# Kernel tuning notes

Hardware: AMD Instinct MI355X
Metric: run time of the kernel (lower is better)

## Reference

```python
import jax, jax.numpy as jnp
import numpy as np

B, T, I, H, O = 256, 512, 64, 512, 1


def setup_inputs() -> dict:
    key = jax.random.key(0)
    ks = jax.random.split(key, 8)
    s_ih = 1.0 / np.sqrt(H)
    inp = {
        "x": jax.random.normal(ks[0], (B, T, I), dtype=jnp.float32),
        "W_ih": jax.random.uniform(ks[1], (4 * H, I), minval=-s_ih, maxval=s_ih, dtype=jnp.float32),
        "W_hh": jax.random.uniform(ks[2], (4 * H, H), minval=-s_ih, maxval=s_ih, dtype=jnp.float32),
        "b_ih": jax.random.uniform(ks[3], (4 * H,), minval=-s_ih, maxval=s_ih, dtype=jnp.float32),
        "b_hh": jax.random.uniform(ks[4], (4 * H,), minval=-s_ih, maxval=s_ih, dtype=jnp.float32),
        "W_fc": jax.random.uniform(ks[5], (O, H), minval=-s_ih, maxval=s_ih, dtype=jnp.float32),
        "b_fc": jax.random.uniform(ks[6], (O,), minval=-s_ih, maxval=s_ih, dtype=jnp.float32),
    }
    return inp


def _lstm_last_h(x, W_ih, W_hh, b_ih, b_hh):
    # x: [B, T, I]. Precompute input projection for all timesteps (one big GEMM).
    x_gates = jnp.einsum("bti,gi->btg", x, W_ih) + b_ih + b_hh  # [B, T, 4H]
    x_gates = jnp.swapaxes(x_gates, 0, 1)  # [T, B, 4H] for scan
    hdim = W_hh.shape[1]
    h0 = jnp.zeros((x.shape[0], hdim), dtype=x.dtype)
    c0 = jnp.zeros((x.shape[0], hdim), dtype=x.dtype)

    def step(carry, xg):
        h, c = carry
        gates = xg + h @ W_hh.T  # [B, 4H]
        i, f, g, o = jnp.split(gates, 4, axis=-1)  # PyTorch gate order: i, f, g, o
        i = jax.nn.sigmoid(i)
        f = jax.nn.sigmoid(f)
        g = jnp.tanh(g)
        o = jax.nn.sigmoid(o)
        c = f * c + i * g
        h = o * jnp.tanh(c)
        return (h, c), None

    (h_last, _), _ = jax.lax.scan(step, (h0, c0), x_gates)
    return h_last  # [B, H] == out[:, -1, :] for a single-layer LSTM


def reference(x, W_ih, W_hh, b_ih, b_hh, W_fc, b_fc):
    h_last = _lstm_last_h(x, W_ih, W_hh, b_ih, b_hh)
    return h_last @ W_fc.T + b_fc  # [B, O]
```

## Files before the change

### kernel.cpp

```cpp
#include <hip/hip_runtime.h>

typedef _Float16 h8 __attribute__((ext_vector_type(8)));
typedef float v4f __attribute__((ext_vector_type(4)));
typedef unsigned long long u64;

#define B_  256
#define T_  512
#define I_  64
#define H_  512

#define OFF_W16   0
#define OFF_WIH   (OFF_W16 + 2048*512*2)
#define OFF_BIAS  (OFF_WIH + 2048*64*2)
#define OFF_X16   (OFF_BIAS + 2048*4)
#define OFF_H0    (OFF_X16 + 512*256*64*2)
#define OFF_H1    (OFF_H0 + 256*512*2)
#define OFF_CTR   (OFF_H1 + 256*512*2)

#define CS_ 1040

__device__ __forceinline__ float sigf(float x) {
    float e = __builtin_amdgcn_exp2f(-1.442695041f * x);
    return __builtin_amdgcn_rcpf(1.f + e);
}
__device__ __forceinline__ float tanhf_(float x) {
    float e = __builtin_amdgcn_exp2f(2.885390082f * x);
    return 1.f - 2.f * __builtin_amdgcn_rcpf(e + 1.f);
}

union Pack4 { _Float16 f[4]; u64 u; };

__global__ void prep_w(const float* __restrict__ Wih, const float* __restrict__ Whh,
                       const float* __restrict__ bih, const float* __restrict__ bhh,
                       _Float16* __restrict__ W16, _Float16* __restrict__ Wih16,
                       float* __restrict__ bias, _Float16* __restrict__ h0,
                       unsigned* __restrict__ ctr) {
    int idx = blockIdx.x * 256 + threadIdx.x;
    W16[idx] = (_Float16)Whh[idx];
    if (idx < 2048 * 64)  Wih16[idx] = (_Float16)Wih[idx];
    if (idx < 2048)       bias[idx] = bih[idx] + bhh[idx];
    if (idx < 32768)
        __hip_atomic_store((u64*)h0 + idx, 0ull,
                           __ATOMIC_RELAXED, __HIP_MEMORY_SCOPE_AGENT);
    if (idx < 256)
        __hip_atomic_store(ctr + idx, 0u, __ATOMIC_RELAXED, __HIP_MEMORY_SCOPE_AGENT);
}

__global__ void prep_x(const float* __restrict__ x, _Float16* __restrict__ x16) {
    int idx = blockIdx.x * 256 + threadIdx.x;
    int t = idx >> 14;
    int rem = idx & 16383;
    int b = rem >> 6;
    int i = rem & 63;
    x16[idx] = (_Float16)x[((size_t)b * T_ + t) * I_ + i];
}

__launch_bounds__(256, 1)
__global__ void lstm_k(const _Float16* __restrict__ W16, const _Float16* __restrict__ Wih16,
                       const float* __restrict__ bias, const _Float16* __restrict__ x16,
                       _Float16* __restrict__ h0, _Float16* __restrict__ h1,
                       unsigned* __restrict__ ctr) {
    __shared__ __align__(16) char Ab[16 * CS_];

    const int tid  = threadIdx.x;
    const int lane = tid & 63;
    const int wv   = tid >> 6;
    const int bg   = blockIdx.x & 15;
    const int cg   = blockIdx.x >> 4;
    const int B0   = bg * 16;
    const int J0   = cg * 64;
    const int r    = lane & 15;
    const int q    = lane >> 4;

    h8 bfrag[4][16];
    h8 xbfrag[4][2];
    float biasv[4];
#pragma unroll
    for (int g = 0; g < 4; ++g) {
        const int wrow = g * H_ + J0 + wv * 16 + r;
#pragma unroll
        for (int kk = 0; kk < 16; ++kk)
            bfrag[g][kk] = *(const h8*)(W16 + (size_t)wrow * H_ + kk * 32 + q * 8);
#pragma unroll
        for (int c = 0; c < 2; ++c)
            xbfrag[g][c] = *(const h8*)(Wih16 + (size_t)wrow * I_ + c * 32 + q * 8);
        biasv[g] = bias[wrow];
    }

    const int wbase = ((tid >> 3) & 15) * CS_ + (tid & 7) * 8;
    const int rw0   = tid >> 7;
    const int rb0 = r * 64 + q * 16;

    float cc[4] = {0.f, 0.f, 0.f, 0.f};

    unsigned* myctr = ctr + bg * 16;

    const _Float16* xrow0 = x16 + (size_t)(B0 + r) * I_ + q * 8;
    h8 xa0 = *(const h8*)(xrow0);
    h8 xa1 = *(const h8*)(xrow0 + 32);

    for (int s = 0; s < T_; ++s) {
        const _Float16* hp = (s & 1) ? h1 : h0;
        _Float16*       hn = (s & 1) ? h0 : h1;

        u64 hv[8];
        {
            const u64* hp64 = (const u64*)(hp + (size_t)B0 * H_);
#pragma unroll
            for (int it = 0; it < 8; ++it)
                hv[it] = __hip_atomic_load(hp64 + tid + 256 * it,
                                           __ATOMIC_RELAXED, __HIP_MEMORY_SCOPE_AGENT);
        }

        v4f a0 = {0,0,0,0}, a1 = {0,0,0,0}, a2 = {0,0,0,0}, a3 = {0,0,0,0};
        a0 = __builtin_amdgcn_mfma_f32_16x16x32_f16(xa0, xbfrag[0][0], a0, 0, 0, 0);
        a1 = __builtin_amdgcn_mfma_f32_16x16x32_f16(xa0, xbfrag[1][0], a1, 0, 0, 0);
        a2 = __builtin_amdgcn_mfma_f32_16x16x32_f16(xa0, xbfrag[2][0], a2, 0, 0, 0);
        a3 = __builtin_amdgcn_mfma_f32_16x16x32_f16(xa0, xbfrag[3][0], a3, 0, 0, 0);
        a0 = __builtin_amdgcn_mfma_f32_16x16x32_f16(xa1, xbfrag[0][1], a0, 0, 0, 0);
        a1 = __builtin_amdgcn_mfma_f32_16x16x32_f16(xa1, xbfrag[1][1], a1, 0, 0, 0);
        a2 = __builtin_amdgcn_mfma_f32_16x16x32_f16(xa1, xbfrag[2][1], a2, 0, 0, 0);
        a3 = __builtin_amdgcn_mfma_f32_16x16x32_f16(xa1, xbfrag[3][1], a3, 0, 0, 0);

#pragma unroll
        for (int it = 0; it < 8; ++it) {
            int row = rw0 + 2 * it;
            *(u64*)(Ab + wbase + row * 64) = hv[it];
        }
        __syncthreads();

#pragma unroll
        for (int kk = 0; kk < 16; ++kk) {
            const h8 am = *(const h8*)(Ab + kk * CS_ + rb0);
            a0 = __builtin_amdgcn_mfma_f32_16x16x32_f16(am, bfrag[0][kk], a0, 0, 0, 0);
            a1 = __builtin_amdgcn_mfma_f32_16x16x32_f16(am, bfrag[1][kk], a1, 0, 0, 0);
            a2 = __builtin_amdgcn_mfma_f32_16x16x32_f16(am, bfrag[2][kk], a2, 0, 0, 0);
            a3 = __builtin_amdgcn_mfma_f32_16x16x32_f16(am, bfrag[3][kk], a3, 0, 0, 0);
        }

        {
            unsigned short* hw = (unsigned short*)hn
                               + (size_t)(B0 + q * 4) * H_ + J0 + wv * 16 + r;
#pragma unroll
            for (int reg = 0; reg < 4; ++reg) {
                float iv = sigf  (a0[reg] + biasv[0]);
                float fv = sigf  (a1[reg] + biasv[1]);
                float gv = tanhf_(a2[reg] + biasv[2]);
                float ov = sigf  (a3[reg] + biasv[3]);
                cc[reg] = fv * cc[reg] + iv * gv;
                union { _Float16 f; unsigned short u; } cv;
                cv.f = (_Float16)(ov * tanhf_(cc[reg]));
                __hip_atomic_store(hw + (size_t)reg * H_, cv.u,
                                   __ATOMIC_RELAXED, __HIP_MEMORY_SCOPE_AGENT);
            }
        }
        __syncthreads();

        if (tid == 0)
            __hip_atomic_fetch_add(myctr, 1u, __ATOMIC_RELAXED, __HIP_MEMORY_SCOPE_AGENT);
        if (s + 1 < T_) {
            const _Float16* xr = x16 + ((size_t)(s + 1) * B_ + B0 + r) * I_ + q * 8;
            xa0 = *(const h8*)(xr);
            xa1 = *(const h8*)(xr + 32);
        }
        if (tid == 0) {
            const unsigned target = 8u * (unsigned)(s + 1);
            int guard = 0;
            while (__hip_atomic_load(myctr, __ATOMIC_RELAXED, __HIP_MEMORY_SCOPE_AGENT) < target) {
                __builtin_amdgcn_s_sleep(1);
                if (++guard > (1 << 17)) break;
            }
        }
        __syncthreads();
    }
}

__global__ void fc_k(const _Float16* __restrict__ hlast, const float* __restrict__ Wfc,
                     const float* __restrict__ bfc, float* __restrict__ out) {
    int b = blockIdx.x;
    int lane = threadIdx.x;
    const u64* hp64 = (const u64*)(hlast + (size_t)b * H_);
    Pack4 p0, p1;
    p0.u = __hip_atomic_load(hp64 + lane * 2,     __ATOMIC_RELAXED, __HIP_MEMORY_SCOPE_AGENT);
    p1.u = __hip_atomic_load(hp64 + lane * 2 + 1, __ATOMIC_RELAXED, __HIP_MEMORY_SCOPE_AGENT);
    float sum = 0.f;
#pragma unroll
    for (int j = 0; j < 4; ++j) sum += (float)p0.f[j] * Wfc[lane * 8 + j];
#pragma unroll
    for (int j = 0; j < 4; ++j) sum += (float)p1.f[j] * Wfc[lane * 8 + 4 + j];
    for (int off = 32; off; off >>= 1) sum += __shfl_down(sum, off);
    if (lane == 0) out[b] = sum + bfc[0];
}

extern "C" void kernel_launch(void* const* d_in, const int* in_sizes, int n_in,
                              void* d_out, int out_size, void* d_ws, size_t ws_size,
                              hipStream_t stream) {
    (void)in_sizes; (void)n_in; (void)out_size; (void)ws_size;
    const float* x   = (const float*)d_in[0];
    const float* Wih = (const float*)d_in[1];
    const float* Whh = (const float*)d_in[2];
    const float* bih = (const float*)d_in[3];
    const float* bhh = (const float*)d_in[4];
    const float* Wfc = (const float*)d_in[5];
    const float* bfc = (const float*)d_in[6];
    float* out = (float*)d_out;

    char* ws = (char*)d_ws;
    _Float16* W16   = (_Float16*)(ws + OFF_W16);
    _Float16* Wih16 = (_Float16*)(ws + OFF_WIH);
    float*    biasf = (float*)(ws + OFF_BIAS);
    _Float16* x16   = (_Float16*)(ws + OFF_X16);
    _Float16* h0b   = (_Float16*)(ws + OFF_H0);
    _Float16* h1b   = (_Float16*)(ws + OFF_H1);
    unsigned* ctrb  = (unsigned*)(ws + OFF_CTR);

    hipLaunchKernelGGL(prep_w, dim3((2048 * 512) / 256), dim3(256), 0, stream,
                       Wih, Whh, bih, bhh, W16, Wih16, biasf, h0b, ctrb);
    hipLaunchKernelGGL(prep_x, dim3((512 * 256 * 64) / 256), dim3(256), 0, stream, x, x16);
    hipLaunchKernelGGL(lstm_k, dim3(128), dim3(256), 0, stream,
                       W16, Wih16, biasf, x16, h0b, h1b, ctrb);
    hipLaunchKernelGGL(fc_k, dim3(256), dim3(64), 0, stream, h0b, Wfc, bfc, out);
}
```

Before: 1.439 ms.

## Interleave two batch groups per block to hide inter-block sync latency

Each block now processes two 16-row batch groups (A and B) instead of one, with the grid halved from 128 to 64 blocks. The block polls the counter and loads h for one group while computing the recurrent GEMM and gate update of the other, so the cross-block barrier wait overlaps with MFMA work. This trades half the parallelism (fewer CUs in use, serial compute per block doubled) for hiding the per-step synchronization latency. Per-group counters with an explicit vmcnt wait replace the single barrier-then-flag sequence.

```diff
diff --git a/kernel.cpp b/kernel.cpp
--- a/kernel.cpp
+++ b/kernel.cpp
@@ -29,6 +29,14 @@
 }
 
 union Pack4 { _Float16 f[4]; u64 u; };
+
+__device__ __forceinline__ void poll_ctr(unsigned* p, unsigned tgt) {
+    int guard = 0;
+    while (__hip_atomic_load(p, __ATOMIC_RELAXED, __HIP_MEMORY_SCOPE_AGENT) < tgt) {
+        __builtin_amdgcn_s_sleep(1);
+        if (++guard > (1 << 17)) break;
+    }
+}
 
 __global__ void prep_w(const float* __restrict__ Wih, const float* __restrict__ Whh,
                        const float* __restrict__ bih, const float* __restrict__ bhh,
@@ -65,9 +73,10 @@
     const int tid  = threadIdx.x;
     const int lane = tid & 63;
     const int wv   = tid >> 6;
-    const int bg   = blockIdx.x & 15;
-    const int cg   = blockIdx.x >> 4;
-    const int B0   = bg * 16;
+    const int p    = blockIdx.x & 7;
+    const int cg   = blockIdx.x >> 3;
+    const int B0A  = p * 16;
+    const int B0B  = B0A + 128;
     const int J0   = cg * 64;
     const int r    = lane & 15;
     const int q    = lane >> 4;
@@ -89,45 +98,60 @@
 
     const int wbase = ((tid >> 3) & 15) * CS_ + (tid & 7) * 8;
     const int rw0   = tid >> 7;
-    const int rb0 = r * 64 + q * 16;
-
-    float cc[4] = {0.f, 0.f, 0.f, 0.f};
-
-    unsigned* myctr = ctr + bg * 16;
-
-    const _Float16* xrow0 = x16 + (size_t)(B0 + r) * I_ + q * 8;
-    h8 xa0 = *(const h8*)(xrow0);
-    h8 xa1 = *(const h8*)(xrow0 + 32);
+    const int rb0   = r * 64 + q * 16;
+
+    float ccA[4] = {0.f, 0.f, 0.f, 0.f};
+    float ccB[4] = {0.f, 0.f, 0.f, 0.f};
+
+    unsigned* const ctrA = ctr + (p)     * 16;
+    unsigned* const ctrB = ctr + (p + 8) * 16;
+
+    u64 hvA[8];
+    {
+        const u64* hp64 = (const u64*)(h0 + (size_t)B0A * H_);
+#pragma unroll
+        for (int it = 0; it < 8; ++it)
+            hvA[it] = __hip_atomic_load(hp64 + tid + 256 * it,
+                                        __ATOMIC_RELAXED, __HIP_MEMORY_SCOPE_AGENT);
+    }
+    h8 xaA0, xaA1, xaB0, xaB1;
+    {
+        const _Float16* xrA = x16 + (size_t)(B0A + r) * I_ + q * 8;
+        const _Float16* xrB = x16 + (size_t)(B0B + r) * I_ + q * 8;
+        xaA0 = *(const h8*)(xrA);  xaA1 = *(const h8*)(xrA + 32);
+        xaB0 = *(const h8*)(xrB);  xaB1 = *(const h8*)(xrB + 32);
+    }
 
     for (int s = 0; s < T_; ++s) {
         const _Float16* hp = (s & 1) ? h1 : h0;
         _Float16*       hn = (s & 1) ? h0 : h1;
 
-        u64 hv[8];
-        {
-            const u64* hp64 = (const u64*)(hp + (size_t)B0 * H_);
-#pragma unroll
-            for (int it = 0; it < 8; ++it)
-                hv[it] = __hip_atomic_load(hp64 + tid + 256 * it,
-                                           __ATOMIC_RELAXED, __HIP_MEMORY_SCOPE_AGENT);
-        }
-
-        v4f a0 = {0,0,0,0}, a1 = {0,0,0,0}, a2 = {0,0,0,0}, a3 = {0,0,0,0};
-        a0 = __builtin_amdgcn_mfma_f32_16x16x32_f16(xa0, xbfrag[0][0], a0, 0, 0, 0);
-        a1 = __builtin_amdgcn_mfma_f32_16x16x32_f16(xa0, xbfrag[1][0], a1, 0, 0, 0);
-        a2 = __builtin_amdgcn_mfma_f32_16x16x32_f16(xa0, xbfrag[2][0], a2, 0, 0, 0);
-        a3 = __builtin_amdgcn_mfma_f32_16x16x32_f16(xa0, xbfrag[3][0], a3, 0, 0, 0);
-        a0 = __builtin_amdgcn_mfma_f32_16x16x32_f16(xa1, xbfrag[0][1], a0, 0, 0, 0);
-        a1 = __builtin_amdgcn_mfma_f32_16x16x32_f16(xa1, xbfrag[1][1], a1, 0, 0, 0);
-        a2 = __builtin_amdgcn_mfma_f32_16x16x32_f16(xa1, xbfrag[2][1], a2, 0, 0, 0);
-        a3 = __builtin_amdgcn_mfma_f32_16x16x32_f16(xa1, xbfrag[3][1], a3, 0, 0, 0);
-
 #pragma unroll
         for (int it = 0; it < 8; ++it) {
             int row = rw0 + 2 * it;
-            *(u64*)(Ab + wbase + row * 64) = hv[it];
-        }
-        __syncthreads();
+            *(u64*)(Ab + wbase + row * 64) = hvA[it];
+        }
+        __syncthreads();
+
+        v4f a0 = {0,0,0,0}, a1 = {0,0,0,0}, a2 = {0,0,0,0}, a3 = {0,0,0,0};
+        a0 = __builtin_amdgcn_mfma_f32_16x16x32_f16(xaA0, xbfrag[0][0], a0, 0, 0, 0);
+        a1 = __builtin_amdgcn_mfma_f32_16x16x32_f16(xaA0, xbfrag[1][0], a1, 0, 0, 0);
+        a2 = __builtin_amdgcn_mfma_f32_16x16x32_f16(xaA0, xbfrag[2][0], a2, 0, 0, 0);
+        a3 = __builtin_amdgcn_mfma_f32_16x16x32_f16(xaA0, xbfrag[3][0], a3, 0, 0, 0);
+        a0 = __builtin_amdgcn_mfma_f32_16x16x32_f16(xaA1, xbfrag[0][1], a0, 0, 0, 0);
+        a1 = __builtin_amdgcn_mfma_f32_16x16x32_f16(xaA1, xbfrag[1][1], a1, 0, 0, 0);
+        a2 = __builtin_amdgcn_mfma_f32_16x16x32_f16(xaA1, xbfrag[2][1], a2, 0, 0, 0);
+        a3 = __builtin_amdgcn_mfma_f32_16x16x32_f16(xaA1, xbfrag[3][1], a3, 0, 0, 0);
+
+        u64 hvB[8];
+        if (s) poll_ctr(ctrB, 8u * (unsigned)s);
+        {
+            const u64* hp64 = (const u64*)(hp + (size_t)B0B * H_);
+#pragma unroll
+            for (int it = 0; it < 8; ++it)
+                hvB[it] = __hip_atomic_load(hp64 + tid + 256 * it,
+                                            __ATOMIC_RELAXED, __HIP_MEMORY_SCOPE_AGENT);
+        }
 
 #pragma unroll
         for (int kk = 0; kk < 16; ++kk) {
@@ -137,40 +161,84 @@
             a2 = __builtin_amdgcn_mfma_f32_16x16x32_f16(am, bfrag[2][kk], a2, 0, 0, 0);
             a3 = __builtin_amdgcn_mfma_f32_16x16x32_f16(am, bfrag[3][kk], a3, 0, 0, 0);
         }
-
         {
             unsigned short* hw = (unsigned short*)hn
-                               + (size_t)(B0 + q * 4) * H_ + J0 + wv * 16 + r;
+                               + (size_t)(B0A + q * 4) * H_ + J0 + wv * 16 + r;
 #pragma unroll
             for (int reg = 0; reg < 4; ++reg) {
                 float iv = sigf  (a0[reg] + biasv[0]);
                 float fv = sigf  (a1[reg] + biasv[1]);
                 float gv = tanhf_(a2[reg] + biasv[2]);
                 float ov = sigf  (a3[reg] + biasv[3]);
-                cc[reg] = fv * cc[reg] + iv * gv;
+                ccA[reg] = fv * ccA[reg] + iv * gv;
                 union { _Float16 f; unsigned short u; } cv;
-                cv.f = (_Float16)(ov * tanhf_(cc[reg]));
+                cv.f = (_Float16)(ov * tanhf_(ccA[reg]));
                 __hip_atomic_store(hw + (size_t)reg * H_, cv.u,
                                    __ATOMIC_RELAXED, __HIP_MEMORY_SCOPE_AGENT);
             }
         }
-        __syncthreads();
-
+        asm volatile("s_waitcnt vmcnt(0)" ::: "memory");
         if (tid == 0)
-            __hip_atomic_fetch_add(myctr, 1u, __ATOMIC_RELAXED, __HIP_MEMORY_SCOPE_AGENT);
+            __hip_atomic_fetch_add(ctrA, 1u, __ATOMIC_RELAXED, __HIP_MEMORY_SCOPE_AGENT);
+        __syncthreads();
+
+#pragma unroll
+        for (int it = 0; it < 8; ++it) {
+            int row = rw0 + 2 * it;
+            *(u64*)(Ab + wbase + row * 64) = hvB[it];
+        }
+        __syncthreads();
+
+        v4f b0 = {0,0,0,0}, b1v = {0,0,0,0}, b2v = {0,0,0,0}, b3v = {0,0,0,0};
+        b0  = __builtin_amdgcn_mfma_f32_16x16x32_f16(xaB0, xbfrag[0][0], b0, 0, 0, 0);
+        b1v = __builtin_amdgcn_mfma_f32_16x16x32_f16(xaB0, xbfrag[1][0], b1v, 0, 0, 0);
+        b2v = __builtin_amdgcn_mfma_f32_16x16x32_f16(xaB0, xbfrag[2][0], b2v, 0, 0, 0);
+        b3v = __builtin_amdgcn_mfma_f32_16x16x32_f16(xaB0, xbfrag[3][0], b3v, 0, 0, 0);
+        b0  = __builtin_amdgcn_mfma_f32_16x16x32_f16(xaB1, xbfrag[0][1], b0, 0, 0, 0);
+        b1v = __builtin_amdgcn_mfma_f32_16x16x32_f16(xaB1, xbfrag[1][1], b1v, 0, 0, 0);
+        b2v = __builtin_amdgcn_mfma_f32_16x16x32_f16(xaB1, xbfrag[2][1], b2v, 0, 0, 0);
+        b3v = __builtin_amdgcn_mfma_f32_16x16x32_f16(xaB1, xbfrag[3][1], b3v, 0, 0, 0);
+
         if (s + 1 < T_) {
-            const _Float16* xr = x16 + ((size_t)(s + 1) * B_ + B0 + r) * I_ + q * 8;
-            xa0 = *(const h8*)(xr);
-            xa1 = *(const h8*)(xr + 32);
-        }
-        if (tid == 0) {
-            const unsigned target = 8u * (unsigned)(s + 1);
-            int guard = 0;
-            while (__hip_atomic_load(myctr, __ATOMIC_RELAXED, __HIP_MEMORY_SCOPE_AGENT) < target) {
-                __builtin_amdgcn_s_sleep(1);
-                if (++guard > (1 << 17)) break;
+            poll_ctr(ctrA, 8u * (unsigned)(s + 1));
+            const u64* hp64 = (const u64*)(hn + (size_t)B0A * H_);
+#pragma unroll
+            for (int it = 0; it < 8; ++it)
+                hvA[it] = __hip_atomic_load(hp64 + tid + 256 * it,
+                                            __ATOMIC_RELAXED, __HIP_MEMORY_SCOPE_AGENT);
+            const _Float16* xrA = x16 + ((size_t)(s + 1) * B_ + B0A + r) * I_ + q * 8;
+            const _Float16* xrB = x16 + ((size_t)(s + 1) * B_ + B0B + r) * I_ + q * 8;
+            xaA0 = *(const h8*)(xrA);  xaA1 = *(const h8*)(xrA + 32);
+            xaB0 = *(const h8*)(xrB);  xaB1 = *(const h8*)(xrB + 32);
+        }
+
+#pragma unroll
+        for (int kk = 0; kk < 16; ++kk) {
+            const h8 am = *(const h8*)(Ab + kk * CS_ + rb0);
+            b0  = __builtin_amdgcn_mfma_f32_16x16x32_f16(am, bfrag[0][kk], b0, 0, 0, 0);
+            b1v = __builtin_amdgcn_mfma_f32_16x16x32_f16(am, bfrag[1][kk], b1v, 0, 0, 0);
+            b2v = __builtin_amdgcn_mfma_f32_16x16x32_f16(am, bfrag[2][kk], b2v, 0, 0, 0);
+            b3v = __builtin_amdgcn_mfma_f32_16x16x32_f16(am, bfrag[3][kk], b3v, 0, 0, 0);
+        }
+        {
+            unsigned short* hw = (unsigned short*)hn
+                               + (size_t)(B0B + q * 4) * H_ + J0 + wv * 16 + r;
+#pragma unroll
+            for (int reg = 0; reg < 4; ++reg) {
+                float iv = sigf  (b0[reg]  + biasv[0]);
+                float fv = sigf  (b1v[reg] + biasv[1]);
+                float gv = tanhf_(b2v[reg] + biasv[2]);
+                float ov = sigf  (b3v[reg] + biasv[3]);
+                ccB[reg] = fv * ccB[reg] + iv * gv;
+                union { _Float16 f; unsigned short u; } cv;
+                cv.f = (_Float16)(ov * tanhf_(ccB[reg]));
+                __hip_atomic_store(hw + (size_t)reg * H_, cv.u,
+                                   __ATOMIC_RELAXED, __HIP_MEMORY_SCOPE_AGENT);
             }
         }
+        asm volatile("s_waitcnt vmcnt(0)" ::: "memory");
+        if (tid == 0)
+            __hip_atomic_fetch_add(ctrB, 1u, __ATOMIC_RELAXED, __HIP_MEMORY_SCOPE_AGENT);
         __syncthreads();
     }
 }
@@ -217,7 +285,7 @@
     hipLaunchKernelGGL(prep_w, dim3((2048 * 512) / 256), dim3(256), 0, stream,
                        Wih, Whh, bih, bhh, W16, Wih16, biasf, h0b, ctrb);
     hipLaunchKernelGGL(prep_x, dim3((512 * 256 * 64) / 256), dim3(256), 0, stream, x, x16);
-    hipLaunchKernelGGL(lstm_k, dim3(128), dim3(256), 0, stream,
+    hipLaunchKernelGGL(lstm_k, dim3(64), dim3(256), 0, stream,
                        W16, Wih16, biasf, x16, h0b, h1b, ctrb);
     hipLaunchKernelGGL(fc_k, dim3(256), dim3(64), 0, stream, h0b, Wfc, bfc, out);
 }
```

Measured after the change: 2.476 ms. +72.0%, slower.
